# Performance work log

Hardware: AMD Instinct MI355X
Metric: run time of the kernel (lower is better)

Reference implementation:

```python
import jax, jax.numpy as jnp
import numpy as np


def _three_nn(xyz1, xyz2):
    # xyz1: [B,N1,3], xyz2: [B,N2,3]
    # Squared euclidean distances, as in the original three_nn CUDA/TF op.
    d2 = (jnp.sum(xyz1 * xyz1, axis=-1)[:, :, None]
          + jnp.sum(xyz2 * xyz2, axis=-1)[:, None, :]
          - 2.0 * jnp.einsum('bnd,bmd->bnm', xyz1, xyz2))  # [B,N1,N2]
    neg_vals, idx = jax.lax.top_k(-d2, 3)                 # 3 smallest
    return -neg_vals, idx                                  # dist [B,N1,3], idx [B,N1,3]


def reference(xyz1, xyz2, points1, points2, w1, w2):
    dist, idx = _three_nn(xyz1, xyz2)
    dist = jnp.maximum(dist, 1e-10)
    inv = 1.0 / dist                                       # [B,N1,3]
    weight = inv / jnp.sum(inv, axis=2, keepdims=True)     # [B,N1,3]

    B = points2.shape[0]
    b_idx = jnp.arange(B)[:, None, None]
    gathered = points2[b_idx, idx]                         # [B,N1,3,C2]
    interpolated = jnp.einsum('bnk,bnkc->bnc', weight, gathered)  # [B,N1,C2]

    new_points = jnp.concatenate([interpolated, points1], axis=2)  # [B,N1,C2+C1]

    # 1x1 conv MLP = per-point matmul; bn=False, activation=relu on all layers
    h = jax.nn.relu(jnp.einsum('bnc,cf->bnf', new_points, w1))
    h = jax.nn.relu(jnp.einsum('bnc,cf->bnf', h, w2))
    return h


def setup_inputs() -> dict:
    key = jax.random.key(0)
    k1, k2, k3, k4, k5, k6 = jax.random.split(key, 6)
    B, N1, N2, C1, C2 = 4, 8192, 2048, 128, 256
    xyz1 = jax.random.normal(k1, (B, N1, 3), dtype=jnp.float32)
    xyz2 = jax.random.normal(k2, (B, N2, 3), dtype=jnp.float32)
    points1 = jax.random.normal(k3, (B, N1, C1), dtype=jnp.float32)
    points2 = jax.random.normal(k4, (B, N2, C2), dtype=jnp.float32)
    # glorot-normal-ish init for the 1x1 conv kernels
    w1 = jax.random.normal(k5, (C2 + C1, 256), dtype=jnp.float32) * (2.0 / (C2 + C1 + 256)) ** 0.5
    w2 = jax.random.normal(k6, (256, 256), dtype=jnp.float32) * (2.0 / (256 + 256)) ** 0.5
    return {"xyz1": xyz1, "xyz2": xyz2, "points1": points1, "points2": points2, "w1": w1, "w2": w2}
```

## Files before the change

### kernel.cpp

```cpp
#include <hip/hip_runtime.h>
#include <stdint.h>

typedef unsigned short u16;
typedef unsigned int   u32;

#define NB 4
#define N1 8192
#define N2 2048
#define C1 128
#define C2 256
#define KK1 384
#define FF 256
#define TM 64
#define NTHR 1024
#define NCH 16
#define PTSA 768
#define SUBA (PTSA / NCH)
#define PTSB 1280
#define SUBB (PTSB / NCH)
#define NPRE 8
#define TILES_PER_B (N1 / TM)
#define APAD 400
#define HPAD 272
#define NKT1 (KK1 / 32)
#define NKT2 (FF / 32)

typedef short short8 __attribute__((ext_vector_type(8)));
typedef float floatx4 __attribute__((ext_vector_type(4)));
typedef float f32x2  __attribute__((ext_vector_type(2)));
typedef u32   u32x4  __attribute__((ext_vector_type(4)));

union ABFrag { u32 u[4]; short8 v; u32x4 q; };

__device__ __forceinline__ u16 f2b(float f) {
    u32 x = __float_as_uint(f);
    return (u16)((x + 0x7FFFu + ((x >> 16) & 1u)) >> 16);
}
__device__ __forceinline__ u32 pack2(float a, float b) {
    u32 r;
    asm("v_cvt_pk_bf16_f32 %0, %1, %2" : "=v"(r) : "v"(a), "v"(b));
    return r;
}

#define INS3(d, ix, d0, d1, d2, i0, i1, i2)                         \
    {                                                               \
        float n0 = fminf(d, d0);                                    \
        float n1 = __builtin_amdgcn_fmed3f(d, d0, d1);              \
        float n2 = __builtin_amdgcn_fmed3f(d, d1, d2);              \
        bool c0 = d < d0, c1 = d < d1, c2 = d < d2;                 \
        int t01 = c0 ? i0 : ix;                                     \
        i0      = c0 ? ix : i0;                                     \
        int t12 = c1 ? i1 : t01;                                    \
        i1      = c1 ? t01 : i1;                                    \
        i2      = c2 ? t12 : i2;                                    \
        d0 = n0; d1 = n1; d2 = n2;                                  \
    }

#define DPAIR(f0, f1, qx, qy, qz, s1, out)                          \
    {                                                               \
        _Pragma("clang fp contract(off)")                           \
        f32x2 qx2 = {qx, qx}, qy2 = {qy, qy}, qz2 = {qz, qz};       \
        f32x2 s1v = {s1, s1};                                       \
        f32x2 nx = {f0.x, f0.y}, ny = {f0.z, f0.w};                 \
        f32x2 nz = {f1.x, f1.y}, ss = {f1.z, f1.w};                 \
        f32x2 u  = qx2 * nx;                                        \
        f32x2 v  = qy2 * ny;                                        \
        f32x2 w  = u + v;                                           \
        f32x2 z2 = qz2 * nz;                                        \
        f32x2 t  = w + z2;                                          \
        f32x2 s12 = s1v + ss;                                       \
        out = s12 + t;                                              \
    }

__global__ __launch_bounds__(1024) void prep_kernel(
    const float* __restrict__ w1, const float* __restrict__ w2,
    const float* __restrict__ xyz2,
    u32x4* __restrict__ w1F, u32x4* __restrict__ w2F, float* __restrict__ xq)
{
    __shared__ float lds[32][257];
    const int tid = threadIdx.x;
    const int blk = blockIdx.x;

    if (blk < NKT1 + NKT2) {
        const bool isw1 = blk < NKT1;
        const int  kt   = isw1 ? blk : blk - NKT1;
        const float* src = (isw1 ? w1 : w2) + (size_t)kt * 32 * FF;
        #pragma unroll
        for (int i = 0; i < 8; ++i) {
            int e = tid + i * 1024;
            lds[e >> 8][e & 255] = src[e];
        }
        __syncthreads();
        const int nt = tid >> 6, lane = tid & 63;
        const int n  = nt * 16 + (lane & 15);
        const int k0 = (lane >> 4) * 8;
        ABFrag f;
        f.u[0] = pack2(lds[k0 + 0][n], lds[k0 + 1][n]);
        f.u[1] = pack2(lds[k0 + 2][n], lds[k0 + 3][n]);
        f.u[2] = pack2(lds[k0 + 4][n], lds[k0 + 5][n]);
        f.u[3] = pack2(lds[k0 + 6][n], lds[k0 + 7][n]);
        if (isw1) w1F[(size_t)(nt * NKT1 + kt) * 64 + lane] = f.q;
        else      w2F[(size_t)(nt * NKT2 + kt) * 64 + lane] = f.q;
        return;
    }

    int i = (blk - NKT1 - NKT2) * 1024 + tid;
    const float* q = xyz2 + (size_t)i * 3;
    float x = q[0], y = q[1], z = q[2];
    float s2 = __fadd_rn(__fadd_rn(__fmul_rn(x,x), __fmul_rn(y,y)), __fmul_rn(z,z));
    int p = i >> 1, e = i & 1;
    float* rec = xq + (size_t)p * 8;
    rec[0 + e] = -2.0f * x;
    rec[2 + e] = -2.0f * y;
    rec[4 + e] = -2.0f * z;
    rec[6 + e] = s2;
}

__global__ __launch_bounds__(NTHR, 8) void fp_fused_kernel(
    const float* __restrict__ xyz1, const float* __restrict__ p1,
    const float* __restrict__ p2,
    const u32x4* __restrict__ w1F,  const u32x4* __restrict__ w2F,
    const float4* __restrict__ xq,  float* __restrict__ out)
{
    __shared__ int   s_idx[TM][3];
    __shared__ float s_wt[TM][3];
    __shared__ float s_m[TM][8];
    __shared__ float s_pd[NCH * TM * 3];
    __shared__ int   s_pi[NCH * TM * 3];
    __shared__ __align__(16) char s_buf[TM * APAD * 2];

    const int tid = threadIdx.x;
    const int b   = blockIdx.x / TILES_PER_B;
    const int t0  = (blockIdx.x % TILES_PER_B) * TM;
    u16* A = (u16*)s_buf;

    const int c4 = (tid & 31) * 4, r32 = tid >> 5;
    float4 pv0 = *(const float4*)(p1 + ((size_t)b * N1 + t0 + r32) * C1 + c4);
    float4 pv1 = *(const float4*)(p1 + ((size_t)b * N1 + t0 + r32 + 32) * C1 + c4);

    const int r  = tid & 63;
    const int ch = __builtin_amdgcn_readfirstlane(tid >> 6);

    const float* q = xyz1 + ((size_t)b * N1 + t0 + r) * 3;
    const float qx = q[0], qy = q[1], qz = q[2];
    const float s1 = __fadd_rn(__fadd_rn(__fmul_rn(qx,qx), __fmul_rn(qy,qy)), __fmul_rn(qz,qz));

    {
        const float4* cb = xq + ((size_t)b * (N2 / 2) + ch * (SUBA / 2)) * 2;
        float bd0 = 3e38f, bd1 = 3e38f, bd2 = 3e38f;
        int   bi0 = -1, bi1 = -1, bi2 = -1;
        const int j0 = ch * SUBA;
        #pragma unroll 8
        for (int jj = 0; jj < SUBA / 2; ++jj) {
            float4 f0 = cb[2 * jj];
            float4 f1 = cb[2 * jj + 1];
            f32x2 dpair;
            DPAIR(f0, f1, qx, qy, qz, s1, dpair);
            #pragma unroll
            for (int e = 0; e < 2; ++e) {
                float d = dpair[e];
                int   j = j0 + 2 * jj + e;
                INS3(d, j, bd0, bd1, bd2, bi0, bi1, bi2);
            }
        }
        const int o = (ch * TM + r) * 3;
        s_pd[o+0] = bd0; s_pd[o+1] = bd1; s_pd[o+2] = bd2;
        s_pi[o+0] = bi0; s_pi[o+1] = bi1; s_pi[o+2] = bi2;
    }

    const float4* cbB = xq + ((size_t)b * (N2 / 2) + (PTSA / 2) + ch * (SUBB / 2)) * 2;
    f32x2 preB[NPRE];
    #pragma unroll
    for (int jj = 0; jj < NPRE; ++jj) {
        float4 f0 = cbB[2 * jj];
        float4 f1 = cbB[2 * jj + 1];
        DPAIR(f0, f1, qx, qy, qz, s1, preB[jj]);
    }

    {
        u32* w0 = (u32*)(A + r32 * APAD + 256 + c4);
        w0[0] = pack2(pv0.x, pv0.y);
        w0[1] = pack2(pv0.z, pv0.w);
        u32* w1p = (u32*)(A + (r32 + 32) * APAD + 256 + c4);
        w1p[0] = pack2(pv1.x, pv1.y);
        w1p[1] = pack2(pv1.z, pv1.w);
    }
    __syncthreads();

    if (tid < 256) {
        const int row = tid & 63, grp = tid >> 6;
        float d0 = 3e38f, d1 = 3e38f, d2 = 3e38f;
        int   i0 = -1, i1 = -1, i2 = -1;
        #pragma unroll
        for (int c = 0; c < 4; ++c) {
            const int o = ((grp * 4 + c) * TM + row) * 3;
            #pragma unroll
            for (int k = 0; k < 3; ++k) {
                float d = s_pd[o + k]; int ix = s_pi[o + k];
                INS3(d, ix, d0, d1, d2, i0, i1, i2);
            }
        }
        float* sg = (float*)(s_buf + row * (APAD * 2) + grp * 32);
        sg[0] = d0; sg[1] = d1; sg[2] = d2;
        sg[3] = __int_as_float(i0); sg[4] = __int_as_float(i1); sg[5] = __int_as_float(i2);
    }
    __syncthreads();

    if (tid < TM) {
        float d0 = 3e38f, d1 = 3e38f, d2 = 3e38f;
        int   i0 = -1, i1 = -1, i2 = -1;
        #pragma unroll
        for (int g = 0; g < 4; ++g) {
            const float* sg = (const float*)(s_buf + tid * (APAD * 2) + g * 32);
            #pragma unroll
            for (int k = 0; k < 3; ++k) {
                float d = sg[k]; int ix = __float_as_int(sg[3 + k]);
                INS3(d, ix, d0, d1, d2, i0, i1, i2);
            }
        }
        s_m[tid][0] = d0; s_m[tid][1] = d1; s_m[tid][2] = d2;
        s_m[tid][4] = __int_as_float(i0);
        s_m[tid][5] = __int_as_float(i1);
        s_m[tid][6] = __int_as_float(i2);
    }
    __syncthreads();

    {
        const float bound = s_m[r][2];
        float bd0 = bound, bd1 = bound, bd2 = bound;
        int   bi0 = -1, bi1 = -1, bi2 = -1;
        const int j0 = PTSA + ch * SUBB;
        #pragma unroll
        for (int jj = 0; jj < NPRE; ++jj) {
            f32x2 dpair = preB[jj];
            if (__any((dpair.x < bd2) || (dpair.y < bd2))) {
                #pragma unroll
                for (int e = 0; e < 2; ++e) {
                    float d = dpair[e];
                    int   j = j0 + 2 * jj + e;
                    INS3(d, j, bd0, bd1, bd2, bi0, bi1, bi2);
                }
            }
        }
        #pragma unroll 4
        for (int jj = NPRE; jj < SUBB / 2; ++jj) {
            float4 f0 = cbB[2 * jj];
            float4 f1 = cbB[2 * jj + 1];
            f32x2 dpair;
            DPAIR(f0, f1, qx, qy, qz, s1, dpair);
            if (__any((dpair.x < bd2) || (dpair.y < bd2))) {
                #pragma unroll
                for (int e = 0; e < 2; ++e) {
                    float d = dpair[e];
                    int   j = j0 + 2 * jj + e;
                    INS3(d, j, bd0, bd1, bd2, bi0, bi1, bi2);
                }
            }
        }
        const int o = (ch * TM + r) * 3;
        s_pd[o+0] = bd0; s_pd[o+1] = bd1; s_pd[o+2] = bd2;
        s_pi[o+0] = bi0; s_pi[o+1] = bi1; s_pi[o+2] = bi2;
    }
    __syncthreads();

    if (tid < 256) {
        const int row = tid & 63, grp = tid >> 6;
        float d0 = 3e38f, d1 = 3e38f, d2 = 3e38f;
        int   i0 = -1, i1 = -1, i2 = -1;
        #pragma unroll
        for (int c = 0; c < 4; ++c) {
            const int o = ((grp * 4 + c) * TM + row) * 3;
            #pragma unroll
            for (int k = 0; k < 3; ++k) {
                float d = s_pd[o + k]; int ix = s_pi[o + k];
                INS3(d, ix, d0, d1, d2, i0, i1, i2);
            }
        }
        float* sg = (float*)(s_buf + row * (APAD * 2) + grp * 32);
        sg[0] = d0; sg[1] = d1; sg[2] = d2;
        sg[3] = __int_as_float(i0); sg[4] = __int_as_float(i1); sg[5] = __int_as_float(i2);
    }
    __syncthreads();

    if (tid < TM) {
        float d0 = s_m[tid][0], d1 = s_m[tid][1], d2 = s_m[tid][2];
        int   i0 = __float_as_int(s_m[tid][4]);
        int   i1 = __float_as_int(s_m[tid][5]);
        int   i2 = __float_as_int(s_m[tid][6]);
        #pragma unroll
        for (int g = 0; g < 4; ++g) {
            const float* sg = (const float*)(s_buf + tid * (APAD * 2) + g * 32);
            #pragma unroll
            for (int k = 0; k < 3; ++k) {
                float d = sg[k]; int ix = __float_as_int(sg[3 + k]);
                INS3(d, ix, d0, d1, d2, i0, i1, i2);
            }
        }
        d0 = fmaxf(d0, 1e-10f); d1 = fmaxf(d1, 1e-10f); d2 = fmaxf(d2, 1e-10f);
        float v0 = 1.0f / d0, v1 = 1.0f / d1, v2 = 1.0f / d2;
        float s  = 1.0f / (v0 + v1 + v2);
        s_wt[tid][0] = v0 * s; s_wt[tid][1] = v1 * s; s_wt[tid][2] = v2 * s;
        s_idx[tid][0] = i0; s_idx[tid][1] = i1; s_idx[tid][2] = i2;
    }
    __syncthreads();

    const int lane = tid & 63;
    const int wv   = tid >> 6;
    const int lr   = lane & 15;
    const int lg   = lane >> 4;
    const int kb8  = lg * 8;
    const int rowH = (wv & 1) * 32;
    const int colB = (wv >> 1) * 32;
    const int nt0  = (wv >> 1) * 2;

    ABFrag bfc1[2];
    bfc1[0].q = w1F[(size_t)((nt0 + 0) * NKT1) * 64 + lane];
    bfc1[1].q = w1F[(size_t)((nt0 + 1) * NKT1) * 64 + lane];

    {
        const float* pb = p2 + (size_t)b * N2 * C2;
        const int col4 = (tid & 63) * 4;
        const int wvr  = tid >> 6;
        float4 a0[2], a1[2], a2[2];
        {
            int rr = wvr;
            a0[0] = *(const float4*)(pb + (size_t)s_idx[rr][0] * C2 + col4);
            a1[0] = *(const float4*)(pb + (size_t)s_idx[rr][1] * C2 + col4);
            a2[0] = *(const float4*)(pb + (size_t)s_idx[rr][2] * C2 + col4);
        }
        #pragma unroll
        for (int m = 0; m < 4; ++m) {
            int cur = m & 1, nxt = cur ^ 1;
            if (m < 3) {
                int rn = wvr + (m + 1) * 16;
                a0[nxt] = *(const float4*)(pb + (size_t)s_idx[rn][0] * C2 + col4);
                a1[nxt] = *(const float4*)(pb + (size_t)s_idx[rn][1] * C2 + col4);
                a2[nxt] = *(const float4*)(pb + (size_t)s_idx[rn][2] * C2 + col4);
            }
            int rr = wvr + m * 16;
            float w0 = s_wt[rr][0], w1v = s_wt[rr][1], w2v = s_wt[rr][2];
            float e0 = w0 * a0[cur].x + w1v * a1[cur].x + w2v * a2[cur].x;
            float e1 = w0 * a0[cur].y + w1v * a1[cur].y + w2v * a2[cur].y;
            float e2 = w0 * a0[cur].z + w1v * a1[cur].z + w2v * a2[cur].z;
            float e3 = w0 * a0[cur].w + w1v * a1[cur].w + w2v * a2[cur].w;
            u32* w = (u32*)(A + rr * APAD + col4);
            w[0] = pack2(e0, e1);
            w[1] = pack2(e2, e3);
        }
    }
    __syncthreads();

    int id1[4], id2[4];
    {
        u16 rbf = f2b((float)lr);
        u16 c32 = f2b(1.0f / 32.0f);
        ABFrag pa, pc;
        u32 ra = (u32)rbf | ((u32)rbf << 16);
        u32 rc = (u32)c32 | ((u32)c32 << 16);
        pa.u[0] = pa.u[1] = pa.u[2] = pa.u[3] = ra;
        pc.u[0] = pc.u[1] = pc.u[2] = pc.u[3] = rc;
        floatx4 z = {0.f, 0.f, 0.f, 0.f};
        floatx4 D1 = __builtin_amdgcn_mfma_f32_16x16x32_bf16(pa.v, pc.v, z, 0, 0, 0);
        floatx4 D2 = __builtin_amdgcn_mfma_f32_16x16x32_bf16(pc.v, pa.v, z, 0, 0, 0);
        #pragma unroll
        for (int g = 0; g < 4; ++g) { id1[g] = (int)(D1[g] + 0.5f); id2[g] = (int)(D2[g] + 0.5f); }
    }

    floatx4 acc[2][2];
    #pragma unroll
    for (int i = 0; i < 2; ++i)
        #pragma unroll
        for (int j = 0; j < 2; ++j) acc[i][j] = floatx4{0.f, 0.f, 0.f, 0.f};
    {
        #pragma unroll 2
        for (int kk = 0; kk < NKT1; ++kk) {
            int kn = (kk + 1 < NKT1) ? kk + 1 : kk;
            ABFrag bfn[2];
            bfn[0].q = w1F[(size_t)((nt0 + 0) * NKT1 + kn) * 64 + lane];
            bfn[1].q = w1F[(size_t)((nt0 + 1) * NKT1 + kn) * 64 + lane];
            ABFrag a[2];
            #pragma unroll
            for (int rt = 0; rt < 2; ++rt)
                a[rt].q = *(const u32x4*)(A + (rowH + rt * 16 + lr) * APAD + kk * 32 + kb8);
            #pragma unroll
            for (int rt = 0; rt < 2; ++rt)
                #pragma unroll
                for (int ct = 0; ct < 2; ++ct)
                    acc[rt][ct] = __builtin_amdgcn_mfma_f32_16x16x32_bf16(a[rt].v, bfc1[ct].v, acc[rt][ct], 0, 0, 0);
            bfc1[0] = bfn[0]; bfc1[1] = bfn[1];
        }
    }
    ABFrag bfc2[2];
    bfc2[0].q = w2F[(size_t)((nt0 + 0) * NKT2) * 64 + lane];
    bfc2[1].q = w2F[(size_t)((nt0 + 1) * NKT2) * 64 + lane];
    __syncthreads();

    u16* H = (u16*)s_buf;
    #pragma unroll
    for (int rt = 0; rt < 2; ++rt)
        #pragma unroll
        for (int ct = 0; ct < 2; ++ct)
            #pragma unroll
            for (int g = 0; g < 4; ++g) {
                int row = rowH + rt * 16 + id1[g];
                int col = colB + ct * 16 + id2[g];
                H[row * HPAD + col] = f2b(fmaxf(acc[rt][ct][g], 0.0f));
            }
    __syncthreads();

    floatx4 acc2[2][2];
    #pragma unroll
    for (int i = 0; i < 2; ++i)
        #pragma unroll
        for (int j = 0; j < 2; ++j) acc2[i][j] = floatx4{0.f, 0.f, 0.f, 0.f};
    {
        #pragma unroll 2
        for (int kk = 0; kk < NKT2; ++kk) {
            int kn = (kk + 1 < NKT2) ? kk + 1 : kk;
            ABFrag bfn[2];
            bfn[0].q = w2F[(size_t)((nt0 + 0) * NKT2 + kn) * 64 + lane];
            bfn[1].q = w2F[(size_t)((nt0 + 1) * NKT2 + kn) * 64 + lane];
            ABFrag a[2];
            #pragma unroll
            for (int rt = 0; rt < 2; ++rt)
                a[rt].q = *(const u32x4*)(H + (rowH + rt * 16 + lr) * HPAD + kk * 32 + kb8);
            #pragma unroll
            for (int rt = 0; rt < 2; ++rt)
                #pragma unroll
                for (int ct = 0; ct < 2; ++ct)
                    acc2[rt][ct] = __builtin_amdgcn_mfma_f32_16x16x32_bf16(a[rt].v, bfc2[ct].v, acc2[rt][ct], 0, 0, 0);
            bfc2[0] = bfn[0]; bfc2[1] = bfn[1];
        }
    }

    float* ob = out + ((size_t)b * N1 + t0) * FF;
    #pragma unroll
    for (int rt = 0; rt < 2; ++rt)
        #pragma unroll
        for (int ct = 0; ct < 2; ++ct)
            #pragma unroll
            for (int g = 0; g < 4; ++g) {
                int row = rowH + rt * 16 + id1[g];
                int col = colB + ct * 16 + id2[g];
                ob[(size_t)row * FF + col] = fmaxf(acc2[rt][ct][g], 0.0f);
            }
}

extern "C" void kernel_launch(void* const* d_in, const int* in_sizes, int n_in,
                              void* d_out, int out_size, void* d_ws, size_t ws_size,
                              hipStream_t stream)
{
    (void)in_sizes; (void)n_in; (void)out_size; (void)ws_size;
    const float* xyz1 = (const float*)d_in[0];
    const float* xyz2 = (const float*)d_in[1];
    const float* p1   = (const float*)d_in[2];
    const float* p2   = (const float*)d_in[3];
    const float* w1   = (const float*)d_in[4];
    const float* w2   = (const float*)d_in[5];
    float* out = (float*)d_out;

    u32x4* w1F = (u32x4*)d_ws;
    u32x4* w2F = w1F + 16 * NKT1 * 64;
    float* xqw = (float*)(w2F + 16 * NKT2 * 64);

    prep_kernel<<<NKT1 + NKT2 + (NB * N2 / 1024), 1024, 0, stream>>>(
        w1, w2, xyz2, w1F, w2F, xqw);
    fp_fused_kernel<<<NB * TILES_PER_B, NTHR, 0, stream>>>(
        xyz1, p1, p2, w1F, w2F, (const float4*)xqw, out);
}
```

Baseline: 59.29 us.

## Split fused kernel into separate KNN and GEMM kernels

Splits the fused kernel in two. A 1024-thread KNN kernel finds the three neighbours and writes the weights and indices into spare columns of the output buffer. A 512-thread GEMM kernel reads them back, gathers and interpolates, then runs both MLP layers with a larger per-wave register tile (4x2 MFMA tiles). The aim is to give each phase its own occupancy and thread shape, and to let the KNN kernel skip the large LDS staging buffer. In exchange it adds a second launch and a global round trip through scratch space in the output, which the GEMM kernel's final store overwrites.

After: 73.59 us. +24.1%, slower.

```diff
diff --git a/kernel.cpp b/kernel.cpp
--- a/kernel.cpp
+++ b/kernel.cpp
@@ -12,7 +12,6 @@
 #define KK1 384
 #define FF 256
 #define TM 64
-#define NTHR 1024
 #define NCH 16
 #define PTSA 768
 #define SUBA (PTSA / NCH)
@@ -24,6 +23,7 @@
 #define HPAD 272
 #define NKT1 (KK1 / 32)
 #define NKT2 (FF / 32)
+#define RECC 248
 
 typedef short short8 __attribute__((ext_vector_type(8)));
 typedef float floatx4 __attribute__((ext_vector_type(4)));
@@ -116,27 +116,18 @@
     rec[6 + e] = s2;
 }
 
-__global__ __launch_bounds__(NTHR, 8) void fp_fused_kernel(
-    const float* __restrict__ xyz1, const float* __restrict__ p1,
-    const float* __restrict__ p2,
-    const u32x4* __restrict__ w1F,  const u32x4* __restrict__ w2F,
-    const float4* __restrict__ xq,  float* __restrict__ out)
+__global__ __launch_bounds__(1024, 8) void knn_kernel(
+    const float* __restrict__ xyz1, const float4* __restrict__ xq,
+    float* __restrict__ out)
 {
-    __shared__ int   s_idx[TM][3];
-    __shared__ float s_wt[TM][3];
     __shared__ float s_m[TM][8];
     __shared__ float s_pd[NCH * TM * 3];
     __shared__ int   s_pi[NCH * TM * 3];
-    __shared__ __align__(16) char s_buf[TM * APAD * 2];
+    __shared__ float s_g[TM][4][8];
 
     const int tid = threadIdx.x;
     const int b   = blockIdx.x / TILES_PER_B;
     const int t0  = (blockIdx.x % TILES_PER_B) * TM;
-    u16* A = (u16*)s_buf;
-
-    const int c4 = (tid & 31) * 4, r32 = tid >> 5;
-    float4 pv0 = *(const float4*)(p1 + ((size_t)b * N1 + t0 + r32) * C1 + c4);
-    float4 pv1 = *(const float4*)(p1 + ((size_t)b * N1 + t0 + r32 + 32) * C1 + c4);
 
     const int r  = tid & 63;
     const int ch = __builtin_amdgcn_readfirstlane(tid >> 6);
@@ -176,15 +167,6 @@
         float4 f1 = cbB[2 * jj + 1];
         DPAIR(f0, f1, qx, qy, qz, s1, preB[jj]);
     }
-
-    {
-        u32* w0 = (u32*)(A + r32 * APAD + 256 + c4);
-        w0[0] = pack2(pv0.x, pv0.y);
-        w0[1] = pack2(pv0.z, pv0.w);
-        u32* w1p = (u32*)(A + (r32 + 32) * APAD + 256 + c4);
-        w1p[0] = pack2(pv1.x, pv1.y);
-        w1p[1] = pack2(pv1.z, pv1.w);
-    }
     __syncthreads();
 
     if (tid < 256) {
@@ -200,9 +182,10 @@
                 INS3(d, ix, d0, d1, d2, i0, i1, i2);
             }
         }
-        float* sg = (float*)(s_buf + row * (APAD * 2) + grp * 32);
-        sg[0] = d0; sg[1] = d1; sg[2] = d2;
-        sg[3] = __int_as_float(i0); sg[4] = __int_as_float(i1); sg[5] = __int_as_float(i2);
+        s_g[row][grp][0] = d0; s_g[row][grp][1] = d1; s_g[row][grp][2] = d2;
+        s_g[row][grp][3] = __int_as_float(i0);
+        s_g[row][grp][4] = __int_as_float(i1);
+        s_g[row][grp][5] = __int_as_float(i2);
     }
     __syncthreads();
 
@@ -211,10 +194,9 @@
         int   i0 = -1, i1 = -1, i2 = -1;
         #pragma unroll
         for (int g = 0; g < 4; ++g) {
-            const float* sg = (const float*)(s_buf + tid * (APAD * 2) + g * 32);
             #pragma unroll
             for (int k = 0; k < 3; ++k) {
-                float d = sg[k]; int ix = __float_as_int(sg[3 + k]);
+                float d = s_g[tid][g][k]; int ix = __float_as_int(s_g[tid][g][3 + k]);
                 INS3(d, ix, d0, d1, d2, i0, i1, i2);
             }
         }
@@ -276,9 +258,10 @@
                 INS3(d, ix, d0, d1, d2, i0, i1, i2);
             }
         }
-        float* sg = (float*)(s_buf + row * (APAD * 2) + grp * 32);
-        sg[0] = d0; sg[1] = d1; sg[2] = d2;
-        sg[3] = __int_as_float(i0); sg[4] = __int_as_float(i1); sg[5] = __int_as_float(i2);
+        s_g[row][grp][0] = d0; s_g[row][grp][1] = d1; s_g[row][grp][2] = d2;
+        s_g[row][grp][3] = __int_as_float(i0);
+        s_g[row][grp][4] = __int_as_float(i1);
+        s_g[row][grp][5] = __int_as_float(i2);
     }
     __syncthreads();
 
@@ -289,33 +272,58 @@
         int   i2 = __float_as_int(s_m[tid][6]);
         #pragma unroll
         for (int g = 0; g < 4; ++g) {
-            const float* sg = (const float*)(s_buf + tid * (APAD * 2) + g * 32);
             #pragma unroll
             for (int k = 0; k < 3; ++k) {
-                float d = sg[k]; int ix = __float_as_int(sg[3 + k]);
+                float d = s_g[tid][g][k]; int ix = __float_as_int(s_g[tid][g][3 + k]);
                 INS3(d, ix, d0, d1, d2, i0, i1, i2);
             }
         }
         d0 = fmaxf(d0, 1e-10f); d1 = fmaxf(d1, 1e-10f); d2 = fmaxf(d2, 1e-10f);
         float v0 = 1.0f / d0, v1 = 1.0f / d1, v2 = 1.0f / d2;
         float s  = 1.0f / (v0 + v1 + v2);
-        s_wt[tid][0] = v0 * s; s_wt[tid][1] = v1 * s; s_wt[tid][2] = v2 * s;
-        s_idx[tid][0] = i0; s_idx[tid][1] = i1; s_idx[tid][2] = i2;
-    }
-    __syncthreads();
-
-    const int lane = tid & 63;
-    const int wv   = tid >> 6;
-    const int lr   = lane & 15;
-    const int lg   = lane >> 4;
-    const int kb8  = lg * 8;
-    const int rowH = (wv & 1) * 32;
-    const int colB = (wv >> 1) * 32;
-    const int nt0  = (wv >> 1) * 2;
-
-    ABFrag bfc1[2];
-    bfc1[0].q = w1F[(size_t)((nt0 + 0) * NKT1) * 64 + lane];
-    bfc1[1].q = w1F[(size_t)((nt0 + 1) * NKT1) * 64 + lane];
+        float* rp = out + ((size_t)(b * N1 + t0 + tid) * FF + RECC);
+        *(float2*)(rp)     = make_float2(v0 * s, v1 * s);
+        *(float2*)(rp + 2) = make_float2(v2 * s, __int_as_float(i0));
+        *(float2*)(rp + 4) = make_float2(__int_as_float(i1), __int_as_float(i2));
+    }
+}
+
+__global__ __launch_bounds__(512, 6) void gemm_kernel(
+    const float* __restrict__ p1, const float* __restrict__ p2,
+    const u32x4* __restrict__ w1F, const u32x4* __restrict__ w2F,
+    float* __restrict__ out)
+{
+    __shared__ int   s_idx[TM][3];
+    __shared__ float s_wt[TM][3];
+    __shared__ __align__(16) char s_buf[TM * APAD * 2];
+
+    const int tid = threadIdx.x;
+    const int b   = blockIdx.x / TILES_PER_B;
+    const int t0  = (blockIdx.x % TILES_PER_B) * TM;
+    u16* A = (u16*)s_buf;
+
+    if (tid < TM) {
+        const float* rp = out + ((size_t)(b * N1 + t0 + tid) * FF + RECC);
+        float2 a0 = *(const float2*)(rp);
+        float2 a1 = *(const float2*)(rp + 2);
+        float2 a2 = *(const float2*)(rp + 4);
+        s_wt[tid][0] = a0.x; s_wt[tid][1] = a0.y; s_wt[tid][2] = a1.x;
+        s_idx[tid][0] = __float_as_int(a1.y);
+        s_idx[tid][1] = __float_as_int(a2.x);
+        s_idx[tid][2] = __float_as_int(a2.y);
+    }
+    {
+        const int c4 = (tid & 31) * 4, r16 = tid >> 5;
+        #pragma unroll
+        for (int rv = 0; rv < 4; ++rv) {
+            int rr = r16 + rv * 16;
+            float4 v = *(const float4*)(p1 + ((size_t)b * N1 + t0 + rr) * C1 + c4);
+            u32* w = (u32*)(A + rr * APAD + 256 + c4);
+            w[0] = pack2(v.x, v.y);
+            w[1] = pack2(v.z, v.w);
+        }
+    }
+    __syncthreads();
 
     {
         const float* pb = p2 + (size_t)b * N2 * C2;
@@ -329,15 +337,15 @@
             a2[0] = *(const float4*)(pb + (size_t)s_idx[rr][2] * C2 + col4);
         }
         #pragma unroll
-        for (int m = 0; m < 4; ++m) {
+        for (int m = 0; m < 8; ++m) {
             int cur = m & 1, nxt = cur ^ 1;
-            if (m < 3) {
-                int rn = wvr + (m + 1) * 16;
+            if (m < 7) {
+                int rn = wvr + (m + 1) * 8;
                 a0[nxt] = *(const float4*)(pb + (size_t)s_idx[rn][0] * C2 + col4);
                 a1[nxt] = *(const float4*)(pb + (size_t)s_idx[rn][1] * C2 + col4);
                 a2[nxt] = *(const float4*)(pb + (size_t)s_idx[rn][2] * C2 + col4);
             }
-            int rr = wvr + m * 16;
+            int rr = wvr + m * 8;
             float w0 = s_wt[rr][0], w1v = s_wt[rr][1], w2v = s_wt[rr][2];
             float e0 = w0 * a0[cur].x + w1v * a1[cur].x + w2v * a2[cur].x;
             float e1 = w0 * a0[cur].y + w1v * a1[cur].y + w2v * a2[cur].y;
@@ -349,6 +357,13 @@
         }
     }
     __syncthreads();
+
+    const int lane = tid & 63;
+    const int wv   = tid >> 6;
+    const int lr   = lane & 15;
+    const int lg   = lane >> 4;
+    const int kb8  = lg * 8;
+    const int nt0  = wv * 2;
 
     int id1[4], id2[4];
     {
@@ -366,82 +381,85 @@
         for (int g = 0; g < 4; ++g) { id1[g] = (int)(D1[g] + 0.5f); id2[g] = (int)(D2[g] + 0.5f); }
     }
 
-    floatx4 acc[2][2];
+    floatx4 acc[4][2];
     #pragma unroll
-    for (int i = 0; i < 2; ++i)
+    for (int i = 0; i < 4; ++i)
         #pragma unroll
         for (int j = 0; j < 2; ++j) acc[i][j] = floatx4{0.f, 0.f, 0.f, 0.f};
     {
+        ABFrag bfc[2];
+        bfc[0].q = w1F[(size_t)((nt0 + 0) * NKT1) * 64 + lane];
+        bfc[1].q = w1F[(size_t)((nt0 + 1) * NKT1) * 64 + lane];
         #pragma unroll 2
         for (int kk = 0; kk < NKT1; ++kk) {
             int kn = (kk + 1 < NKT1) ? kk + 1 : kk;
             ABFrag bfn[2];
             bfn[0].q = w1F[(size_t)((nt0 + 0) * NKT1 + kn) * 64 + lane];
             bfn[1].q = w1F[(size_t)((nt0 + 1) * NKT1 + kn) * 64 + lane];
-            ABFrag a[2];
-            #pragma unroll
-            for (int rt = 0; rt < 2; ++rt)
-                a[rt].q = *(const u32x4*)(A + (rowH + rt * 16 + lr) * APAD + kk * 32 + kb8);
-            #pragma unroll
-            for (int rt = 0; rt < 2; ++rt)
+            ABFrag a[4];
+            #pragma unroll
+            for (int rt = 0; rt < 4; ++rt)
+                a[rt].q = *(const u32x4*)(A + (rt * 16 + lr) * APAD + kk * 32 + kb8);
+            #pragma unroll
+            for (int rt = 0; rt < 4; ++rt)
                 #pragma unroll
                 for (int ct = 0; ct < 2; ++ct)
-                    acc[rt][ct] = __builtin_amdgcn_mfma_f32_16x16x32_bf16(a[rt].v, bfc1[ct].v, acc[rt][ct], 0, 0, 0);
-            bfc1[0] = bfn[0]; bfc1[1] = bfn[1];
-        }
-    }
-    ABFrag bfc2[2];
-    bfc2[0].q = w2F[(size_t)((nt0 + 0) * NKT2) * 64 + lane];
-    bfc2[1].q = w2F[(size_t)((nt0 + 1) * NKT2) * 64 + lane];
+                    acc[rt][ct] = __builtin_amdgcn_mfma_f32_16x16x32_bf16(a[rt].v, bfc[ct].v, acc[rt][ct], 0, 0, 0);
+            bfc[0] = bfn[0]; bfc[1] = bfn[1];
+        }
+    }
     __syncthreads();
 
     u16* H = (u16*)s_buf;
     #pragma unroll
-    for (int rt = 0; rt < 2; ++rt)
+    for (int rt = 0; rt < 4; ++rt)
         #pragma unroll
         for (int ct = 0; ct < 2; ++ct)
             #pragma unroll
             for (int g = 0; g < 4; ++g) {
-                int row = rowH + rt * 16 + id1[g];
-                int col = colB + ct * 16 + id2[g];
+                int row = rt * 16 + id1[g];
+                int col = wv * 32 + ct * 16 + id2[g];
                 H[row * HPAD + col] = f2b(fmaxf(acc[rt][ct][g], 0.0f));
             }
     __syncthreads();
 
-    floatx4 acc2[2][2];
+    floatx4 acc2[4][2];
     #pragma unroll
-    for (int i = 0; i < 2; ++i)
+    for (int i = 0; i < 4; ++i)
         #pragma unroll
         for (int j = 0; j < 2; ++j) acc2[i][j] = floatx4{0.f, 0.f, 0.f, 0.f};
     {
+        ABFrag bfc[2];
+        bfc[0].q = w2F[(size_t)((nt0 + 0) * NKT2) * 64 + lane];
+        bfc[1].q = w2F[(size_t)((nt0 + 1) * NKT2) * 64 + lane];
         #pragma unroll 2
         for (int kk = 0; kk < NKT2; ++kk) {
             int kn = (kk + 1 < NKT2) ? kk + 1 : kk;
             ABFrag bfn[2];
             bfn[0].q = w2F[(size_t)((nt0 + 0) * NKT2 + kn) * 64 + lane];
             bfn[1].q = w2F[(size_t)((nt0 + 1) * NKT2 + kn) * 64 + lane];
-            ABFrag a[2];
-            #pragma unroll
-            for (int rt = 0; rt < 2; ++rt)
-                a[rt].q = *(const u32x4*)(H + (rowH + rt * 16 + lr) * HPAD + kk * 32 + kb8);
-            #pragma unroll
-            for (int rt = 0; rt < 2; ++rt)
+            ABFrag a[4];
+            #pragma unroll
+            for (int rt = 0; rt < 4; ++rt)
+                a[rt].q = *(const u32x4*)(H + (rt * 16 + lr) * HPAD + kk * 32 + kb8);
+            #pragma unroll
+            for (int rt = 0; rt < 4; ++rt)
                 #pragma unroll
                 for (int ct = 0; ct < 2; ++ct)
-                    acc2[rt][ct] = __builtin_amdgcn_mfma_f32_16x16x32_bf16(a[rt].v, bfc2[ct].v, acc2[rt][ct], 0, 0, 0);
-            bfc2[0] = bfn[0]; bfc2[1] = bfn[1];
+                    acc2[rt][ct] = __builtin_amdgcn_mfma_f32_16x16x32_bf16(a[rt].v, bfc[ct].v, acc2[rt][ct], 0, 0, 0);
+            bfc[0] = bfn[0]; bfc[1] = bfn[1];
         }
     }
 
     float* ob = out + ((size_t)b * N1 + t0) * FF;
     #pragma unroll
-    for (int rt = 0; rt < 2; ++rt)
+    for (int rt = 0; rt < 4; ++rt)
         #pragma unroll
         for (int ct = 0; ct < 2; ++ct)
             #pragma unroll
             for (int g = 0; g < 4; ++g) {
-                int row = rowH + rt * 16 + id1[g];
-                int col = colB + ct * 16 + id2[g];
+                int row = rt * 16 + id1[g];
+                int col = wv * 32 + ct * 16 + id2[g];
                 ob[(size_t)row * FF + col] = fmaxf(acc2[rt][ct][g], 0.0f);
             }
 }
@@ -465,6 +483,6 @@
 
     prep_kernel<<<NKT1 + NKT2 + (NB * N2 / 1024), 1024, 0, stream>>>(
         w1, w2, xyz2, w1F, w2F, xqw);
-    fp_fused_kernel<<<NB * TILES_PER_B, NTHR, 0, stream>>>(
-        xyz1, p1, p2, w1F, w2F, (const float4*)xqw, out);
-}
+    knn_kernel<<<NB * TILES_PER_B, 1024, 0, stream>>>(xyz1, (const float4*)xqw, out);
+    gemm_kernel<<<NB * TILES_PER_B, 512, 0, stream>>>(p1, p2, w1F, w2F, out);
+}
```
